# Optimization experiments

Measured on AMD Instinct MI355X. Metric: run time of the kernel, lower is better.

## Reference

```python
import jax, jax.numpy as jnp
import numpy as np

WIDTH = 768
HEAD = 64

def setup_inputs() -> dict:
    key = jax.random.key(0)
    ks = jax.random.split(key, 8)
    x = jax.random.normal(ks[0], (8, 2048, WIDTH), dtype=jnp.float32)
    mask = jax.random.randint(ks[1], (2048, 2048), 0, 2, dtype=jnp.int32)
    s = 1.0 / np.sqrt(WIDTH)
    Wq = jax.random.normal(ks[2], (WIDTH, HEAD), dtype=jnp.float32) * s
    Wk = jax.random.normal(ks[3], (WIDTH, HEAD), dtype=jnp.float32) * s
    Wv = jax.random.normal(ks[4], (WIDTH, HEAD), dtype=jnp.float32) * s
    bq = jax.random.normal(ks[5], (HEAD,), dtype=jnp.float32) * 0.01
    bk = jax.random.normal(ks[6], (HEAD,), dtype=jnp.float32) * 0.01
    bv = jax.random.normal(ks[7], (HEAD,), dtype=jnp.float32) * 0.01
    return {"x": x, "Wq": Wq, "bq": bq, "Wk": Wk, "bk": bk, "Wv": Wv, "bv": bv, "mask": mask}

def reference(x, Wq, bq, Wk, bk, Wv, bv, mask) -> jnp.ndarray:
    # x: [B, N, width]; projections -> [B, N, head]
    Q = jnp.einsum('bnw,wh->bnh', x, Wq) + bq
    K = jnp.einsum('bnw,wh->bnh', x, Wk) + bk
    V = jnp.einsum('bnw,wh->bnh', x, Wv) + bv
    scale = 1.0 / jnp.sqrt(jnp.asarray(Q.shape[-1], dtype=Q.dtype))
    scores = jnp.einsum('bqh,bkh->bqk', Q, K) * scale  # [B, N, N]
    scores = jnp.where(mask == 0, -jnp.inf, scores)
    attn = jax.nn.softmax(scores, axis=-1)
    return jnp.einsum('bqk,bkh->bqh', attn, V)
```

## Files before the change

### kernel.cpp

```cpp
#include <hip/hip_runtime.h>

typedef short  s8v   __attribute__((ext_vector_type(8)));
typedef float  f32x4 __attribute__((ext_vector_type(4)));

#define SEQ 2048
#define WID 768

__device__ __forceinline__ unsigned fbits(float f) {
    union { float f; unsigned u; } v; v.f = f; return v.u;
}
__device__ __forceinline__ float bitsf(unsigned u) {
    union { unsigned u; float f; } v; v.u = u; return v.f;
}
__device__ __forceinline__ unsigned short f2b(float f) {
    unsigned u = fbits(f);
    return (unsigned short)((u + 0x7FFFu + ((u >> 16) & 1u)) >> 16);
}
__device__ __forceinline__ unsigned packRNE(float a, float b) {
    unsigned ta = fbits(a) + 0x7FFFu + ((fbits(a) >> 16) & 1u);
    unsigned tb = fbits(b) + 0x7FFFu + ((fbits(b) >> 16) & 1u);
    return __builtin_amdgcn_perm(tb, ta, 0x07060302u);
}
__device__ __forceinline__ unsigned packTRUNC(float a, float b) {
    return __builtin_amdgcn_perm(fbits(b), fbits(a), 0x07060302u);
}
__device__ __forceinline__ f32x4 zero4() { f32x4 z = {0.f, 0.f, 0.f, 0.f}; return z; }

__device__ __forceinline__ void async16(const unsigned short* g, unsigned short* l) {
    __builtin_amdgcn_global_load_lds(
        (const __attribute__((address_space(1))) unsigned int*)g,
        (__attribute__((address_space(3))) unsigned int*)l, 16, 0, 0);
}

__global__ __launch_bounds__(256) void prep_kernel(
    const int* __restrict__ mask,
    const float* __restrict__ Wq, const float* __restrict__ Wk, const float* __restrict__ Wv,
    unsigned* __restrict__ PM, unsigned short* __restrict__ Wt)
{
    const int tid = threadIdx.x;
    const int blk = blockIdx.x;
    if (blk < 512) {
        const int gid  = blk * 4 + (tid >> 6);
        const int lane = tid & 63, quad = lane >> 4, c = lane & 15;
        const int qb = gid >> 5, kb = gid & 31;
        unsigned w = 0;
        #pragma unroll
        for (int mt = 0; mt < 2; ++mt)
            #pragma unroll
            for (int i = 0; i < 4; ++i) {
                const int q = qb * 32 + mt * 16 + quad * 4 + i;
                const int4 mm = *(const int4*)&mask[(size_t)q * SEQ + kb * 64 + 4 * c];
                if (mm.x) w |= 1u << (mt * 16 + i * 4 + 0);
                if (mm.y) w |= 1u << (mt * 16 + i * 4 + 1);
                if (mm.z) w |= 1u << (mt * 16 + i * 4 + 2);
                if (mm.w) w |= 1u << (mt * 16 + i * 4 + 3);
            }
        PM[(size_t)gid * 64 + lane] = w;
    } else {
        const int cid = (blk - 512) * 256 + tid;
        const int mat = cid / 12288;
        const int rem = cid - mat * 12288;
        const int k = rem >> 4, c4 = rem & 15;
        const float* Wm = (mat == 0) ? Wq : (mat == 1) ? Wk : Wv;
        float4 w = *(const float4*)&Wm[(size_t)k * 64 + c4 * 4];
        float wv4[4] = {w.x, w.y, w.z, w.w};
        #pragma unroll
        for (int j = 0; j < 4; ++j)
            Wt[(size_t)(mat * 64 + c4 * 4 + j) * WID + k] = f2b(wv4[j]);
    }
}

__global__ __launch_bounds__(256, 2) void qkv_proj_kernel(
    const float* __restrict__ x, const unsigned short* __restrict__ Wt,
    const float* __restrict__ bq, const float* __restrict__ bk, const float* __restrict__ bv,
    unsigned short* __restrict__ QF, unsigned short* __restrict__ KF,
    unsigned short* __restrict__ VF)
{
    __shared__ unsigned short St[32][208];

    const int tid = threadIdx.x;
    const int wv = tid >> 6, lane = tid & 63, quad = lane >> 4, c = lane & 15;
    const int rowb = blockIdx.x * 32;
    const int row0 = rowb + (wv >> 1) * 16;
    const int c0   = (wv & 1) * 96;

    float bias[6];
    #pragma unroll
    for (int nt = 0; nt < 6; ++nt) {
        int col = c0 + nt * 16 + c;
        const float* B = (col < 64) ? bq : (col < 128) ? bk : bv;
        bias[nt] = B[col & 63];
    }

    const float* xrow = x + (size_t)(row0 + c) * WID + quad * 8;
    const unsigned short* wbase = Wt + (size_t)quad * 8;

    f32x4 acc[6];
    #pragma unroll
    for (int nt = 0; nt < 6; ++nt) acc[nt] = zero4();

    float4 pxa[3], pxb[3];
    uint4  pw[2][6];
    #pragma unroll
    for (int u = 0; u < 3; ++u) {
        pxa[u] = *(const float4*)&xrow[u * 32];
        pxb[u] = *(const float4*)&xrow[u * 32 + 4];
    }
    #pragma unroll
    for (int u = 0; u < 2; ++u)
        #pragma unroll
        for (int nt = 0; nt < 6; ++nt)
            pw[u][nt] = *(const uint4*)&wbase[(size_t)(c0 + nt * 16 + c) * WID + u * 32];

    #pragma unroll
    for (int kc = 0; kc < 24; ++kc) {
        union { uint4 u; s8v v; } af;
        af.u.x = packRNE(pxa[kc % 3].x, pxa[kc % 3].y);
        af.u.y = packRNE(pxa[kc % 3].z, pxa[kc % 3].w);
        af.u.z = packRNE(pxb[kc % 3].x, pxb[kc % 3].y);
        af.u.w = packRNE(pxb[kc % 3].z, pxb[kc % 3].w);
        union { uint4 u; s8v v; } bf[6];
        #pragma unroll
        for (int nt = 0; nt < 6; ++nt) bf[nt].u = pw[kc & 1][nt];

        if (kc + 3 < 24) {
            pxa[kc % 3] = *(const float4*)&xrow[(kc + 3) * 32];
            pxb[kc % 3] = *(const float4*)&xrow[(kc + 3) * 32 + 4];
        }
        if (kc + 2 < 24) {
            #pragma unroll
            for (int nt = 0; nt < 6; ++nt)
                pw[kc & 1][nt] = *(const uint4*)&wbase[(size_t)(c0 + nt * 16 + c) * WID + (kc + 2) * 32];
        }

        #pragma unroll
        for (int nt = 0; nt < 6; ++nt)
            acc[nt] = __builtin_amdgcn_mfma_f32_16x16x32_bf16(af.v, bf[nt].v, acc[nt], 0, 0, 0);
    }

    #pragma unroll
    for (int nt = 0; nt < 6; ++nt)
        #pragma unroll
        for (int i = 0; i < 4; ++i)
            St[(wv >> 1) * 16 + quad * 4 + i][c0 + nt * 16 + c] = f2b(acc[nt][i] + bias[nt]);
    __syncthreads();

    const int kb  = rowb >> 6;
    const int c0k = (rowb & 63) >> 2;
    const int ks0 = (rowb & 63) >> 5;

    {
        const int qg = (tid >> 7) & 1, ks = (tid >> 6) & 1;
        const int l = tid & 63, qd = l >> 4, cc = l & 15;
        uint4 v = *(uint4*)&St[qg * 16 + cc][ks * 32 + qd * 8];
        *(uint4*)&QF[(((size_t)(rowb >> 4) + qg) * 2 + ks) * 512 + (size_t)l * 8] = v;
    }
    {
        const int ksnt = tid >> 5, u = tid & 31;
        const int ks = ksnt >> 2, nt = ksnt & 3;
        const int qd = u >> 3, cc = u & 7;
        uint4 v = *(uint4*)&St[4 * cc + nt][64 + ks * 32 + qd * 8];
        *(uint4*)&KF[(((size_t)kb * 8 + ksnt) * 64 + qd * 16 + c0k + cc) * 8] = v;
    }
    {
        const int nt = tid >> 6, l = tid & 63, qd = l >> 4, cc = l & 15;
        unsigned short p[8];
        #pragma unroll
        for (int s = 0; s < 8; ++s) p[s] = St[qd * 8 + s][128 + nt * 16 + cc];
        uint4 w;
        w.x = (unsigned)p[0] | ((unsigned)p[1] << 16);
        w.y = (unsigned)p[2] | ((unsigned)p[3] << 16);
        w.z = (unsigned)p[4] | ((unsigned)p[5] << 16);
        w.w = (unsigned)p[6] | ((unsigned)p[7] << 16);
        *(uint4*)&VF[(((size_t)kb * 8 + ks0 * 4 + nt) * 64 + l) * 8] = w;
    }
}

__global__ __launch_bounds__(1024) void attn_kernel(
    const unsigned short* __restrict__ QF, const unsigned short* __restrict__ KF,
    const unsigned short* __restrict__ VF, const unsigned* __restrict__ PM,
    float* __restrict__ out)
{
    __shared__ unsigned short KVk[4][4096];
    __shared__ unsigned short KVv[4][4096];
    __shared__ unsigned short Ps[16][16][72];
    __shared__ float Obuf[64][68];
    __shared__ float Lbuf[64];

    const int tid = threadIdx.x;
    const int wv = tid >> 6, lane = tid & 63, quad = lane >> 4, c = lane & 15;
    const int sl = wv & 3, qg = wv >> 2;
    const int mt = qg & 1;
    const int qt = blockIdx.x, bb = blockIdx.y;

    #pragma unroll
    for (int j = 0; j < 5; ++j) {
        int idx = tid + 1024 * j;
        if (idx < 64 * 68) ((float*)Obuf)[idx] = 0.f;
    }
    if (tid < 64) Lbuf[tid] = 0.f;

    s8v qf[2];
    {
        const size_t qgrp = (size_t)bb * 128 + qt * 4 + qg;
        #pragma unroll
        for (int ks = 0; ks < 2; ++ks)
            qf[ks] = *(const s8v*)&QF[(qgrp * 2 + ks) * 512 + (size_t)lane * 8];
    }

    f32x4 O[4];
    float lro[4];
    #pragma unroll
    for (int nt = 0; nt < 4; ++nt) O[nt] = zero4();
    #pragma unroll
    for (int i = 0; i < 4; ++i) lro[i] = 0.f;

    for (int kt = 0; kt < 8; ++kt) {
        const int kbg = bb * 32 + sl * 8 + kt;
        const unsigned short* bk = KF + (size_t)kbg * 4096;
        const unsigned short* bv = VF + (size_t)kbg * 4096;
        #pragma unroll
        for (int r = 0; r < 2; ++r) {
            const int cn = qg * 2 + r;
            async16(bk + cn * 512 + lane * 8, &KVk[sl][cn * 512]);
            async16(bv + cn * 512 + lane * 8, &KVv[sl][cn * 512]);
        }
        const unsigned pm = PM[(size_t)((qt * 2 + (qg >> 1)) * 32 + sl * 8 + kt) * 64 + lane];
        __syncthreads();

        f32x4 S[4];
        #pragma unroll
        for (int nt = 0; nt < 4; ++nt) S[nt] = zero4();
        #pragma unroll
        for (int ks = 0; ks < 2; ++ks) {
            s8v kfr[4];
            #pragma unroll
            for (int nt = 0; nt < 4; ++nt)
                kfr[nt] = *(const s8v*)&KVk[sl][((ks * 4 + nt) * 64 + lane) * 8];
            #pragma unroll
            for (int nt = 0; nt < 4; ++nt)
                S[nt] = __builtin_amdgcn_mfma_f32_16x16x32_bf16(qf[ks], kfr[nt], S[nt], 0, 0, 0);
        }

        const unsigned pmh = pm >> (mt * 16);
        #pragma unroll
        for (int i = 0; i < 4; ++i) {
            float p4[4];
            #pragma unroll
            for (int nt = 0; nt < 4; ++nt) {
                float e = exp2f(fmaf(S[nt][i], 0.18033688011112042f, -21.640425613334451f));
                p4[nt] = ((pmh >> (i * 4 + nt)) & 1u) ? e : 0.f;
            }
            unsigned u0 = packTRUNC(p4[0], p4[1]);
            unsigned u1 = packTRUNC(p4[2], p4[3]);
            lro[i] += bitsf(u0 << 16) + bitsf(u0 & 0xFFFF0000u)
                    + bitsf(u1 << 16) + bitsf(u1 & 0xFFFF0000u);
            *(uint2*)&Ps[wv][quad * 4 + i][4 * c] = make_uint2(u0, u1);
        }

        #pragma unroll
        for (int ks = 0; ks < 2; ++ks) {
            s8v a = *(const s8v*)&Ps[wv][c][ks * 32 + quad * 8];
            s8v vfr[4];
            #pragma unroll
            for (int nt = 0; nt < 4; ++nt)
                vfr[nt] = *(const s8v*)&KVv[sl][((ks * 4 + nt) * 64 + lane) * 8];
            #pragma unroll
            for (int nt = 0; nt < 4; ++nt)
                O[nt] = __builtin_amdgcn_mfma_f32_16x16x32_bf16(a, vfr[nt], O[nt], 0, 0, 0);
        }
        __syncthreads();
    }

    #pragma unroll
    for (int i = 0; i < 4; ++i) {
        float l = lro[i];
        l += __shfl_xor(l, 1);
        l += __shfl_xor(l, 2);
        l += __shfl_xor(l, 4);
        l += __shfl_xor(l, 8);
        if (c == 0) atomicAdd(&Lbuf[qg * 16 + quad * 4 + i], l);
        #pragma unroll
        for (int nt = 0; nt < 4; ++nt)
            atomicAdd(&Obuf[qg * 16 + quad * 4 + i][nt * 16 + c], O[nt][i]);
    }
    __syncthreads();
    {
        const int r = tid >> 4, d4 = (tid & 15) * 4;
        const float invL = 1.0f / Lbuf[r];
        float4 v = *(float4*)&Obuf[r][d4];
        float4 o = make_float4(v.x * invL, v.y * invL, v.z * invL, v.w * invL);
        *(float4*)&out[((size_t)bb * SEQ + qt * 64 + r) * 64 + d4] = o;
    }
}

extern "C" void kernel_launch(void* const* d_in, const int* in_sizes, int n_in,
                              void* d_out, int out_size, void* d_ws, size_t ws_size,
                              hipStream_t stream)
{
    const float* x    = (const float*)d_in[0];
    const float* Wq   = (const float*)d_in[1];
    const float* bq   = (const float*)d_in[2];
    const float* Wk   = (const float*)d_in[3];
    const float* bk   = (const float*)d_in[4];
    const float* Wv   = (const float*)d_in[5];
    const float* bv   = (const float*)d_in[6];
    const int*   mask = (const int*)d_in[7];
    float* out = (float*)d_out;

    unsigned short* QF = (unsigned short*)d_ws;
    unsigned short* KF = QF + (size_t)16384 * 64;
    unsigned short* VF = KF + (size_t)16384 * 64;
    unsigned short* Wt = VF + (size_t)16384 * 64;
    unsigned*       PM = (unsigned*)(Wt + (size_t)192 * WID);

    prep_kernel<<<656, 256, 0, stream>>>(mask, Wq, Wk, Wv, PM, Wt);
    qkv_proj_kernel<<<512, 256, 0, stream>>>(x, Wt, bq, bk, bv, QF, KF, VF);
    attn_kernel<<<dim3(32, 8), 1024, 0, stream>>>(QF, KF, VF, PM, out);
}
```

Before: 192.5 us.

## Restage x through LDS in projection and double-buffer K tiles in attention

The projection kernel now uses 16-row blocks with twice as many blocks. Each block async-loads its x tile into LDS, converts it to bf16 once, and reads A fragments from LDS instead of converting in registers on every k step. The attention kernel double-buffers K tiles and prefetches the next mask word, loads V fragments straight from global into registers, and drops a barrier per iteration. It also reuses the P buffer's LDS for the output reduction and flattens the grid to 1D. The aim is better overlap and occupancy, at the cost of more LDS traffic and uncached V reads from global.

Result: faster. 188.1 us (-2.3%).

```diff
diff --git a/kernel.cpp b/kernel.cpp
--- a/kernel.cpp
+++ b/kernel.cpp
@@ -27,6 +27,11 @@
 __device__ __forceinline__ f32x4 zero4() { f32x4 z = {0.f, 0.f, 0.f, 0.f}; return z; }
 
 __device__ __forceinline__ void async16(const unsigned short* g, unsigned short* l) {
+    __builtin_amdgcn_global_load_lds(
+        (const __attribute__((address_space(1))) unsigned int*)g,
+        (__attribute__((address_space(3))) unsigned int*)l, 16, 0, 0);
+}
+__device__ __forceinline__ void async16f(const float* g, float* l) {
     __builtin_amdgcn_global_load_lds(
         (const __attribute__((address_space(1))) unsigned int*)g,
         (__attribute__((address_space(3))) unsigned int*)l, 16, 0, 0);
@@ -70,134 +75,138 @@
     }
 }
 
-__global__ __launch_bounds__(256, 2) void qkv_proj_kernel(
+__global__ __launch_bounds__(256, 4) void qkv_proj_kernel(
     const float* __restrict__ x, const unsigned short* __restrict__ Wt,
     const float* __restrict__ bq, const float* __restrict__ bk, const float* __restrict__ bv,
     unsigned short* __restrict__ QF, unsigned short* __restrict__ KF,
     unsigned short* __restrict__ VF)
 {
-    __shared__ unsigned short St[32][208];
+    __shared__ __align__(16) unsigned char SMEM[49152];
+    float (*Xs)[WID]           = (float(*)[WID])SMEM;
+    unsigned short (*Xb)[776]  = (unsigned short(*)[776])(SMEM + 8192);
+    unsigned short (*St)[208]  = (unsigned short(*)[208])SMEM;
 
     const int tid = threadIdx.x;
     const int wv = tid >> 6, lane = tid & 63, quad = lane >> 4, c = lane & 15;
-    const int rowb = blockIdx.x * 32;
-    const int row0 = rowb + (wv >> 1) * 16;
-    const int c0   = (wv & 1) * 96;
-
-    float bias[6];
-    #pragma unroll
-    for (int nt = 0; nt < 6; ++nt) {
-        int col = c0 + nt * 16 + c;
+    const int rowb = blockIdx.x * 16;
+    const int c0w  = wv * 48;
+
+    const float* xsrc = x + (size_t)rowb * WID;
+    #pragma unroll
+    for (int t = 0; t < 12; ++t) {
+        const int d = wv * 12 + t;
+        async16f(xsrc + d * 256 + lane * 4, (float*)SMEM + d * 256);
+    }
+
+    float bias[3];
+    #pragma unroll
+    for (int nt = 0; nt < 3; ++nt) {
+        int col = c0w + nt * 16 + c;
         const float* B = (col < 64) ? bq : (col < 128) ? bk : bv;
         bias[nt] = B[col & 63];
     }
-
-    const float* xrow = x + (size_t)(row0 + c) * WID + quad * 8;
-    const unsigned short* wbase = Wt + (size_t)quad * 8;
-
-    f32x4 acc[6];
-    #pragma unroll
-    for (int nt = 0; nt < 6; ++nt) acc[nt] = zero4();
-
-    float4 pxa[3], pxb[3];
-    uint4  pw[2][6];
-    #pragma unroll
-    for (int u = 0; u < 3; ++u) {
-        pxa[u] = *(const float4*)&xrow[u * 32];
-        pxb[u] = *(const float4*)&xrow[u * 32 + 4];
-    }
+    __syncthreads();
+
+    {
+        const int r = tid >> 4, cc0 = (tid & 15) * 48;
+        float4 f[12];
+        #pragma unroll
+        for (int j = 0; j < 12; ++j) f[j] = *(float4*)&Xs[r][cc0 + 4 * j];
+        __syncthreads();
+        #pragma unroll
+        for (int j = 0; j < 6; ++j) {
+            uint4 w;
+            w.x = packRNE(f[2*j].x,   f[2*j].y);
+            w.y = packRNE(f[2*j].z,   f[2*j].w);
+            w.z = packRNE(f[2*j+1].x, f[2*j+1].y);
+            w.w = packRNE(f[2*j+1].z, f[2*j+1].w);
+            *(uint4*)&Xb[r][cc0 + 8 * j] = w;
+        }
+    }
+    __syncthreads();
+
+    f32x4 acc[3];
+    #pragma unroll
+    for (int nt = 0; nt < 3; ++nt) acc[nt] = zero4();
+
+    uint4 pw[2][3];
     #pragma unroll
     for (int u = 0; u < 2; ++u)
         #pragma unroll
-        for (int nt = 0; nt < 6; ++nt)
-            pw[u][nt] = *(const uint4*)&wbase[(size_t)(c0 + nt * 16 + c) * WID + u * 32];
+        for (int nt = 0; nt < 3; ++nt)
+            pw[u][nt] = *(const uint4*)&Wt[(size_t)(c0w + nt * 16 + c) * WID + u * 32 + quad * 8];
 
     #pragma unroll
     for (int kc = 0; kc < 24; ++kc) {
-        union { uint4 u; s8v v; } af;
-        af.u.x = packRNE(pxa[kc % 3].x, pxa[kc % 3].y);
-        af.u.y = packRNE(pxa[kc % 3].z, pxa[kc % 3].w);
-        af.u.z = packRNE(pxb[kc % 3].x, pxb[kc % 3].y);
-        af.u.w = packRNE(pxb[kc % 3].z, pxb[kc % 3].w);
-        union { uint4 u; s8v v; } bf[6];
-        #pragma unroll
-        for (int nt = 0; nt < 6; ++nt) bf[nt].u = pw[kc & 1][nt];
-
-        if (kc + 3 < 24) {
-            pxa[kc % 3] = *(const float4*)&xrow[(kc + 3) * 32];
-            pxb[kc % 3] = *(const float4*)&xrow[(kc + 3) * 32 + 4];
-        }
+        s8v af = *(const s8v*)&Xb[c][kc * 32 + quad * 8];
+        union { uint4 u; s8v v; } bf[3];
+        #pragma unroll
+        for (int nt = 0; nt < 3; ++nt) bf[nt].u = pw[kc & 1][nt];
         if (kc + 2 < 24) {
             #pragma unroll
-            for (int nt = 0; nt < 6; ++nt)
-                pw[kc & 1][nt] = *(const uint4*)&wbase[(size_t)(c0 + nt * 16 + c) * WID + (kc + 2) * 32];
-        }
-
-        #pragma unroll
-        for (int nt = 0; nt < 6; ++nt)
-            acc[nt] = __builtin_amdgcn_mfma_f32_16x16x32_bf16(af.v, bf[nt].v, acc[nt], 0, 0, 0);
-    }
-
-    #pragma unroll
-    for (int nt = 0; nt < 6; ++nt)
+            for (int nt = 0; nt < 3; ++nt)
+                pw[kc & 1][nt] = *(const uint4*)&Wt[(size_t)(c0w + nt * 16 + c) * WID + (kc + 2) * 32 + quad * 8];
+        }
+        #pragma unroll
+        for (int nt = 0; nt < 3; ++nt)
+            acc[nt] = __builtin_amdgcn_mfma_f32_16x16x32_bf16(af, bf[nt].v, acc[nt], 0, 0, 0);
+    }
+
+    #pragma unroll
+    for (int nt = 0; nt < 3; ++nt)
         #pragma unroll
         for (int i = 0; i < 4; ++i)
-            St[(wv >> 1) * 16 + quad * 4 + i][c0 + nt * 16 + c] = f2b(acc[nt][i] + bias[nt]);
+            St[quad * 4 + i][c0w + nt * 16 + c] = f2b(acc[nt][i] + bias[nt]);
     __syncthreads();
 
     const int kb  = rowb >> 6;
-    const int c0k = (rowb & 63) >> 2;
+    const int q0k = (rowb & 63) >> 2;
     const int ks0 = (rowb & 63) >> 5;
-
-    {
-        const int qg = (tid >> 7) & 1, ks = (tid >> 6) & 1;
-        const int l = tid & 63, qd = l >> 4, cc = l & 15;
-        uint4 v = *(uint4*)&St[qg * 16 + cc][ks * 32 + qd * 8];
-        *(uint4*)&QF[(((size_t)(rowb >> 4) + qg) * 2 + ks) * 512 + (size_t)l * 8] = v;
-    }
-    {
-        const int ksnt = tid >> 5, u = tid & 31;
-        const int ks = ksnt >> 2, nt = ksnt & 3;
-        const int qd = u >> 3, cc = u & 7;
+    const int qd0 = (rowb & 31) >> 3;
+
+    if (tid < 128) {
+        const int ks = tid >> 6, l = tid & 63, qd = l >> 4, cc = l & 15;
+        uint4 v = *(uint4*)&St[cc][ks * 32 + qd * 8];
+        *(uint4*)&QF[(((size_t)(rowb >> 4)) * 2 + ks) * 512 + (size_t)l * 8] = v;
+    } else {
+        const int u = tid - 128;
+        const int ks = u >> 6, nt = (u >> 4) & 3, qd = (u >> 2) & 3, cc = u & 3;
         uint4 v = *(uint4*)&St[4 * cc + nt][64 + ks * 32 + qd * 8];
-        *(uint4*)&KF[(((size_t)kb * 8 + ksnt) * 64 + qd * 16 + c0k + cc) * 8] = v;
-    }
-    {
-        const int nt = tid >> 6, l = tid & 63, qd = l >> 4, cc = l & 15;
+        *(uint4*)&KF[(((size_t)kb * 8 + ks * 4 + nt) * 64 + qd * 16 + q0k + cc) * 8] = v;
+    }
+    if (tid < 128) {
+        const int d = tid >> 1, jj = tid & 1, qd = qd0 + jj;
+        const int nt = d >> 4, cc = d & 15;
         unsigned short p[8];
         #pragma unroll
-        for (int s = 0; s < 8; ++s) p[s] = St[qd * 8 + s][128 + nt * 16 + cc];
+        for (int s = 0; s < 8; ++s) p[s] = St[jj * 8 + s][128 + d];
         uint4 w;
         w.x = (unsigned)p[0] | ((unsigned)p[1] << 16);
         w.y = (unsigned)p[2] | ((unsigned)p[3] << 16);
         w.z = (unsigned)p[4] | ((unsigned)p[5] << 16);
         w.w = (unsigned)p[6] | ((unsigned)p[7] << 16);
-        *(uint4*)&VF[(((size_t)kb * 8 + ks0 * 4 + nt) * 64 + l) * 8] = w;
-    }
-}
-
-__global__ __launch_bounds__(1024) void attn_kernel(
+        *(uint4*)&VF[(((size_t)kb * 8 + ks0 * 4 + nt) * 64 + qd * 16 + cc) * 8] = w;
+    }
+}
+
+__global__ __launch_bounds__(1024, 4) void attn_kernel(
     const unsigned short* __restrict__ QF, const unsigned short* __restrict__ KF,
     const unsigned short* __restrict__ VF, const unsigned* __restrict__ PM,
     float* __restrict__ out)
 {
-    __shared__ unsigned short KVk[4][4096];
-    __shared__ unsigned short KVv[4][4096];
-    __shared__ unsigned short Ps[16][16][72];
-    __shared__ float Obuf[64][68];
+    __shared__ unsigned short KVk[2][4][4096];
+    __shared__ __align__(16) unsigned char PsOb[36864];
     __shared__ float Lbuf[64];
+    unsigned short (*Ps)[16][72] = (unsigned short(*)[16][72])PsOb;
+    float (*Obuf)[68]            = (float(*)[68])PsOb;
 
     const int tid = threadIdx.x;
     const int wv = tid >> 6, lane = tid & 63, quad = lane >> 4, c = lane & 15;
-    const int sl = wv & 3, qg = wv >> 2;
-    const int mt = qg & 1;
-    const int qt = blockIdx.x, bb = blockIdx.y;
-
-    #pragma unroll
-    for (int j = 0; j < 5; ++j) {
-        int idx = tid + 1024 * j;
-        if (idx < 64 * 68) ((float*)Obuf)[idx] = 0.f;
-    }
+    const int sl = wv & 3, qg = wv >> 2, mt = qg & 1;
+    const int blk = blockIdx.x;
+    const int bb = blk & 7, qt = blk >> 3;
+    const size_t qrow0 = (size_t)bb * SEQ + qt * 64;
+
     if (tid < 64) Lbuf[tid] = 0.f;
 
     s8v qf[2];
@@ -215,18 +224,29 @@
     #pragma unroll
     for (int i = 0; i < 4; ++i) lro[i] = 0.f;
 
-    for (int kt = 0; kt < 8; ++kt) {
-        const int kbg = bb * 32 + sl * 8 + kt;
-        const unsigned short* bk = KF + (size_t)kbg * 4096;
-        const unsigned short* bv = VF + (size_t)kbg * 4096;
+    {
+        const size_t kbg = (size_t)bb * 32 + sl * 8;
         #pragma unroll
         for (int r = 0; r < 2; ++r) {
             const int cn = qg * 2 + r;
-            async16(bk + cn * 512 + lane * 8, &KVk[sl][cn * 512]);
-            async16(bv + cn * 512 + lane * 8, &KVv[sl][cn * 512]);
-        }
-        const unsigned pm = PM[(size_t)((qt * 2 + (qg >> 1)) * 32 + sl * 8 + kt) * 64 + lane];
+            async16(KF + kbg * 4096 + cn * 512 + lane * 8, &KVk[0][sl][cn * 512]);
+        }
+    }
+    unsigned pm = PM[(size_t)((qt * 2 + (qg >> 1)) * 32 + sl * 8) * 64 + lane];
+
+    for (int kt = 0; kt < 8; ++kt) {
         __syncthreads();
+
+        if (kt < 7) {
+            const size_t kbg = (size_t)bb * 32 + sl * 8 + kt + 1;
+            #pragma unroll
+            for (int r = 0; r < 2; ++r) {
+                const int cn = qg * 2 + r;
+                async16(KF + kbg * 4096 + cn * 512 + lane * 8, &KVk[(kt + 1) & 1][sl][cn * 512]);
+            }
+        }
+        const unsigned pmN = (kt < 7)
+            ? PM[(size_t)((qt * 2 + (qg >> 1)) * 32 + sl * 8 + kt + 1) * 64 + lane] : 0u;
 
         f32x4 S[4];
         #pragma unroll
@@ -236,11 +256,19 @@
             s8v kfr[4];
             #pragma unroll
             for (int nt = 0; nt < 4; ++nt)
-                kfr[nt] = *(const s8v*)&KVk[sl][((ks * 4 + nt) * 64 + lane) * 8];
+                kfr[nt] = *(const s8v*)&KVk[kt & 1][sl][((ks * 4 + nt) * 64 + lane) * 8];
             #pragma unroll
             for (int nt = 0; nt < 4; ++nt)
                 S[nt] = __builtin_amdgcn_mfma_f32_16x16x32_bf16(qf[ks], kfr[nt], S[nt], 0, 0, 0);
         }
+
+        const size_t kbg = (size_t)bb * 32 + sl * 8 + kt;
+        s8v vf[8];
+        #pragma unroll
+        for (int ks = 0; ks < 2; ++ks)
+            #pragma unroll
+            for (int nt = 0; nt < 4; ++nt)
+                vf[ks * 4 + nt] = *(const s8v*)&VF[(kbg * 8 + ks * 4 + nt) * 512 + (size_t)lane * 8];
 
         const unsigned pmh = pm >> (mt * 16);
         #pragma unroll
@@ -257,21 +285,24 @@
                     + bitsf(u1 << 16) + bitsf(u1 & 0xFFFF0000u);
             *(uint2*)&Ps[wv][quad * 4 + i][4 * c] = make_uint2(u0, u1);
         }
+        pm = pmN;
 
         #pragma unroll
         for (int ks = 0; ks < 2; ++ks) {
             s8v a = *(const s8v*)&Ps[wv][c][ks * 32 + quad * 8];
-            s8v vfr[4];
             #pragma unroll
             for (int nt = 0; nt < 4; ++nt)
-                vfr[nt] = *(const s8v*)&KVv[sl][((ks * 4 + nt) * 64 + lane) * 8];
-            #pragma unroll
-            for (int nt = 0; nt < 4; ++nt)
-                O[nt] = __builtin_amdgcn_mfma_f32_16x16x32_bf16(a, vfr[nt], O[nt], 0, 0, 0);
-        }
-        __syncthreads();
-    }
-
+                O[nt] = __builtin_amdgcn_mfma_f32_16x16x32_bf16(a, vf[ks * 4 + nt], O[nt], 0, 0, 0);
+        }
+    }
+
+    __syncthreads();
+    #pragma unroll
+    for (int j = 0; j < 5; ++j) {
+        int idx = tid + 1024 * j;
+        if (idx < 64 * 68) ((float*)Obuf)[idx] = 0.f;
+    }
+    __syncthreads();
     #pragma unroll
     for (int i = 0; i < 4; ++i) {
         float l = lro[i];
@@ -290,7 +321,7 @@
         const float invL = 1.0f / Lbuf[r];
         float4 v = *(float4*)&Obuf[r][d4];
         float4 o = make_float4(v.x * invL, v.y * invL, v.z * invL, v.w * invL);
-        *(float4*)&out[((size_t)bb * SEQ + qt * 64 + r) * 64 + d4] = o;
+        *(float4*)&out[(qrow0 + r) * 64 + d4] = o;
     }
 }
 
@@ -315,6 +346,6 @@
     unsigned*       PM = (unsigned*)(Wt + (size_t)192 * WID);
 
     prep_kernel<<<656, 256, 0, stream>>>(mask, Wq, Wk, Wv, PM, Wt);
-    qkv_proj_kernel<<<512, 256, 0, stream>>>(x, Wt, bq, bk, bv, QF, KF, VF);
-    attn_kernel<<<dim3(32, 8), 1024, 0, stream>>>(QF, KF, VF, PM, out);
-}
+    qkv_proj_kernel<<<1024, 256, 0, stream>>>(x, Wt, bq, bk, bv, QF, KF, VF);
+    attn_kernel<<<256, 1024, 0, stream>>>(QF, KF, VF, PM, out);
+}
```
